# Kernel tuning notes

Measured on AMD Instinct MI355X. Metric: run time of the kernel, lower is better.

## Reference

```python
import jax, jax.numpy as jnp
import numpy as np

# Dims inferred from the module: conv weight (K=3, C_IN=C+1, C_OUT=C)
K_W = 3
C_OUT = 64
C_IN = C_OUT + 1
B, L = 32, 8192
N_STEPS = 8  # fixed-step RK4 stand-in for odeint(rtol=atol=1e-3) over t in [0,1]


def setup_inputs() -> dict:
    key = jax.random.key(0)
    kx, kw = jax.random.split(key)
    x = jax.random.normal(kx, (B, L, C_OUT), dtype=jnp.float32)
    # lecun_uniform: U(-sqrt(3/fan_in), sqrt(3/fan_in)), fan_in = K_W * C_IN
    limit = float(np.sqrt(3.0 / (K_W * C_IN)))
    w = jax.random.uniform(kw, (K_W, C_IN, C_OUT), dtype=jnp.float32,
                           minval=-limit, maxval=limit)
    b = jnp.zeros((C_OUT,), dtype=jnp.float32)
    return {"x": x, "w": w, "b": b}


def _ode_func(y, t, w, b):
    # concat_t: append a constant-t channel -> (B, L, C+1)
    t_chan = jnp.full(y.shape[:-1] + (1,), 1.0, dtype=y.dtype) * t
    z = jnp.concatenate([y, t_chan], axis=-1)
    z = jax.lax.conv_general_dilated(
        z, w, window_strides=(1,), padding="SAME",
        dimension_numbers=("NWC", "WIO", "NWC"))
    return jax.nn.relu(z + b)


def reference(x, w, b):
    h = jnp.float32(1.0 / N_STEPS)

    def step(y, t0):
        k1 = _ode_func(y, t0, w, b)
        k2 = _ode_func(y + 0.5 * h * k1, t0 + 0.5 * h, w, b)
        k3 = _ode_func(y + 0.5 * h * k2, t0 + 0.5 * h, w, b)
        k4 = _ode_func(y + h * k3, t0 + h, w, b)
        y_next = y + (h / 6.0) * (k1 + 2.0 * k2 + 2.0 * k3 + k4)
        return y_next, None

    ts = jnp.arange(N_STEPS, dtype=jnp.float32) * h
    y_final, _ = jax.lax.scan(step, x, ts)
    return y_final
```

## Files before the change

### kernel.cpp

```cpp
#include <hip/hip_runtime.h>
#include <hip/hip_bf16.h>


#define BB 32
#define LL 8192
#define CC 64
#define TILE 64
#define NROW 80
#define BUFR 82
#define ZST 72
#define YST 66
#define CENT_LO 9
#define CENT_HI 72
#define THREADS 256

typedef __attribute__((ext_vector_type(8))) short bf16x8;
typedef __attribute__((ext_vector_type(4))) float f32x4;

__device__ __forceinline__ unsigned short f2bf_u(float f) {
    __hip_bfloat16 h = __float2bfloat16(f);
    return *reinterpret_cast<unsigned short*>(&h);
}

__launch_bounds__(THREADS, 3)
__global__ void step_kernel(const float* __restrict__ y_in, float* __restrict__ y_out,
                            const float* __restrict__ w, const float* __restrict__ bias,
                            float t0, float h)
{
    __shared__ float ys[BUFR * YST];
    __shared__ unsigned short zA[BUFR * ZST];
    __shared__ unsigned short zB[BUFR * ZST];
    __shared__ float wts[3 * CC];
    __shared__ float bs[CC];

    const int tid = threadIdx.x;
    const int b = blockIdx.y;
    const int l0 = blockIdx.x * TILE;
    const int lane = tid & 63;
    const int wv = tid >> 6;
    const int co0 = wv * 16;
    const int g = lane >> 4;
    const int ml = lane & 15;

    bf16x8 bhi[6], blo[6];
#pragma unroll
    for (int c = 0; c < 6; c++) {
        const int kw = c >> 1;
        const int cbase = (c & 1) * 32 + g * 8;
        const float* wp = w + kw * (65 * CC) + cbase * CC + co0 + ml;
#pragma unroll
        for (int j = 0; j < 8; j++) {
            float v = wp[j * CC];
            unsigned short hi = f2bf_u(v);
            float vhi = __uint_as_float(((unsigned)hi) << 16);
            unsigned short lo = f2bf_u(v - vhi);
            bhi[c][j] = (short)hi;
            blo[c][j] = (short)lo;
        }
    }

    if (tid < 3 * CC) wts[tid] = w[(tid >> 6) * (65 * CC) + CC * CC + (tid & 63)];
    if (tid < CC) bs[tid] = bias[tid];

    if (tid < CC) {
        zA[0 * ZST + tid] = 0; zA[81 * ZST + tid] = 0;
        zB[0 * ZST + tid] = 0; zB[81 * ZST + tid] = 0;
    }

    for (int idx = tid; idx < NROW * 16; idx += THREADS) {
        int r = 1 + (idx >> 4);
        int c4 = (idx & 15) * 4;
        int l = l0 - 9 + r;
        float4 v = make_float4(0.f, 0.f, 0.f, 0.f);
        if (l >= 0 && l < LL)
            v = *reinterpret_cast<const float4*>(y_in + ((size_t)b * LL + l) * CC + c4);
        float* yp = &ys[r * YST + c4];
        yp[0] = v.x; yp[1] = v.y; yp[2] = v.z; yp[3] = v.w;
        unsigned short* zp = &zA[r * ZST + c4];
        zp[0] = f2bf_u(v.x); zp[1] = f2bf_u(v.y);
        zp[2] = f2bf_u(v.z); zp[3] = f2bf_u(v.w);
    }
    __syncthreads();

    const float ca0 = h / 6.f, ca1 = h / 3.f;
    const int co = co0 + ml;
    const float w1t = wts[CC + co], w0t = wts[co], w2t = wts[2 * CC + co];
    const float bv = bs[co];

    float accR[5][4];

#pragma unroll 1
    for (int e = 0; e < 4; e++) {
        const unsigned short* zin = (e & 1) ? zB : zA;
        unsigned short* zout = (e & 1) ? zA : zB;
        const float t = t0 + ((e == 0) ? 0.f : (e == 3) ? h : 0.5f * h);
        const float cacc = (e == 0 || e == 3) ? ca0 : ca1;
        const float cuu = (e == 2) ? h : 0.5f * h;

#pragma unroll
        for (int m = 0; m < 5; m++) {
            const int r0 = 1 + 16 * m;
            f32x4 acc = {0.f, 0.f, 0.f, 0.f};
#pragma unroll
            for (int c = 0; c < 6; c++) {
                const int kw = c >> 1;
                const int zoff = (c & 1) * 32 + g * 8;
                const int row = r0 + ml + kw - 1;
                const bf16x8 a =
                    *reinterpret_cast<const bf16x8*>(&zin[row * ZST + zoff]);
                acc = __builtin_amdgcn_mfma_f32_16x16x32_bf16(a, bhi[c], acc, 0, 0, 0);
                acc = __builtin_amdgcn_mfma_f32_16x16x32_bf16(a, blo[c], acc, 0, 0, 0);
            }
#pragma unroll
            for (int i = 0; i < 4; i++) {
                const int rr = r0 + g * 4 + i;
                const int l = l0 - 9 + rr;
                float wt = w1t;
                if (l > 0) wt += w0t;
                if (l < LL - 1) wt += w2t;
                float k = fmaxf(acc[i] + t * wt + bv, 0.f);
                const float yv = ys[rr * YST + co];
                if (e < 3) {
                    float u = yv + cuu * k;
                    if (l < 0 || l >= LL) u = 0.f;
                    zout[rr * ZST + co] = f2bf_u(u);
                }
                accR[m][i] = ((e == 0) ? yv : accR[m][i]) + cacc * k;
            }
        }
        __syncthreads();
    }

#pragma unroll
    for (int m = 0; m < 5; m++) {
#pragma unroll
        for (int i = 0; i < 4; i++) {
            const int rr = 1 + 16 * m + g * 4 + i;
            if (rr >= CENT_LO && rr <= CENT_HI) {
                const int l = l0 - 9 + rr;
                y_out[((size_t)b * LL + l) * CC + co] = accR[m][i];
            }
        }
    }
}

extern "C" void kernel_launch(void* const* d_in, const int* in_sizes, int n_in,
                              void* d_out, int out_size, void* d_ws, size_t ws_size,
                              hipStream_t stream) {
    const float* x = (const float*)d_in[0];
    const float* w = (const float*)d_in[1];
    const float* bias = (const float*)d_in[2];
    float* out = (float*)d_out;
    float* P0 = (float*)d_ws;
    const float h = 1.0f / 8.0f;

    dim3 grid(LL / TILE, BB), block(THREADS);
    for (int s = 0; s < 8; s++) {
        const float* yin = (s == 0) ? x : ((s & 1) ? P0 : out);
        float* yout = (s & 1) ? out : P0;
        step_kernel<<<grid, block, 0, stream>>>(yin, yout, w, bias, s * h, h);
    }
}
```

Before: 700.7 us.

## Enlarge tile, drop bf16 split-precision, keep y in registers

Each block now covers 120 output rows with a 4-row halo instead of 64 with a 9-row halo, which cuts the redundant halo compute and loads. The hi/lo bf16 split of the weights is dropped, so only one bf16 MFMA runs per product, halving MFMA work but lowering precision. The y values stay in registers instead of a shared-memory fp32 buffer. A manual round-to-nearest-even pack writes two channels at once, and edge handling runs only in boundary blocks. The risk is larger numerical error from the single bf16 weights, which may exceed the tolerance.

```diff
diff --git a/kernel.cpp b/kernel.cpp
--- a/kernel.cpp
+++ b/kernel.cpp
@@ -1,145 +1,155 @@
 #include <hip/hip_runtime.h>
-#include <hip/hip_bf16.h>
 
 
 #define BB 32
 #define LL 8192
 #define CC 64
-#define TILE 64
-#define NROW 80
-#define BUFR 82
+#define TILE 120
+#define NBLK 69
+#define BUFR 130
 #define ZST 72
-#define YST 66
-#define CENT_LO 9
-#define CENT_HI 72
 #define THREADS 256
 
 typedef __attribute__((ext_vector_type(8))) short bf16x8;
 typedef __attribute__((ext_vector_type(4))) float f32x4;
 
-__device__ __forceinline__ unsigned short f2bf_u(float f) {
-    __hip_bfloat16 h = __float2bfloat16(f);
-    return *reinterpret_cast<unsigned short*>(&h);
+__device__ __forceinline__ unsigned bf_rne(float f) {
+    unsigned u = __float_as_uint(f);
+    return u + 0x7fffu + ((u >> 16) & 1u);
 }
+__device__ __forceinline__ unsigned pack_bf16(float a, float b) {
+    return (bf_rne(a) >> 16) | (bf_rne(b) & 0xffff0000u);
+}
+__device__ __forceinline__ short bf16_of(float f) { return (short)(bf_rne(f) >> 16); }
 
 __launch_bounds__(THREADS, 3)
 __global__ void step_kernel(const float* __restrict__ y_in, float* __restrict__ y_out,
                             const float* __restrict__ w, const float* __restrict__ bias,
                             float t0, float h)
 {
-    __shared__ float ys[BUFR * YST];
     __shared__ unsigned short zA[BUFR * ZST];
     __shared__ unsigned short zB[BUFR * ZST];
-    __shared__ float wts[3 * CC];
-    __shared__ float bs[CC];
 
     const int tid = threadIdx.x;
     const int b = blockIdx.y;
     const int l0 = blockIdx.x * TILE;
     const int lane = tid & 63;
     const int wv = tid >> 6;
-    const int co0 = wv * 16;
+    const int ch = wv >> 1;
+    const int bset = wv & 1;
     const int g = lane >> 4;
     const int ml = lane & 15;
+    const int co = ch * 32 + 2 * ml;
+    const bool edge = (blockIdx.x == 0) || (blockIdx.x == NBLK - 1);
 
-    bf16x8 bhi[6], blo[6];
+    if (tid < 64) {
+        zA[tid] = 0; zA[129 * ZST + tid] = 0;
+        zB[tid] = 0; zB[129 * ZST + tid] = 0;
+    }
+
+    bf16x8 Bf[6][2];
 #pragma unroll
     for (int c = 0; c < 6; c++) {
-        const int kw = c >> 1;
-        const int cbase = (c & 1) * 32 + g * 8;
-        const float* wp = w + kw * (65 * CC) + cbase * CC + co0 + ml;
+        const float* wp = w + (c >> 1) * (65 * CC) + (((c & 1) * 32) + g * 8) * CC + co;
 #pragma unroll
         for (int j = 0; j < 8; j++) {
-            float v = wp[j * CC];
-            unsigned short hi = f2bf_u(v);
-            float vhi = __uint_as_float(((unsigned)hi) << 16);
-            unsigned short lo = f2bf_u(v - vhi);
-            bhi[c][j] = (short)hi;
-            blo[c][j] = (short)lo;
+            float2 v = *(const float2*)(wp + j * CC);
+            Bf[c][0][j] = bf16_of(v.x);
+            Bf[c][1][j] = bf16_of(v.y);
         }
     }
+    const float2 wt0 = *(const float2*)(w + 0 * (65 * CC) + CC * CC + co);
+    const float2 wt1 = *(const float2*)(w + 1 * (65 * CC) + CC * CC + co);
+    const float2 wt2 = *(const float2*)(w + 2 * (65 * CC) + CC * CC + co);
+    const float2 bv  = *(const float2*)(bias + co);
 
-    if (tid < 3 * CC) wts[tid] = w[(tid >> 6) * (65 * CC) + CC * CC + (tid & 63)];
-    if (tid < CC) bs[tid] = bias[tid];
-
-    if (tid < CC) {
-        zA[0 * ZST + tid] = 0; zA[81 * ZST + tid] = 0;
-        zB[0 * ZST + tid] = 0; zB[81 * ZST + tid] = 0;
-    }
-
-    for (int idx = tid; idx < NROW * 16; idx += THREADS) {
-        int r = 1 + (idx >> 4);
-        int c4 = (idx & 15) * 4;
-        int l = l0 - 9 + r;
-        float4 v = make_float4(0.f, 0.f, 0.f, 0.f);
-        if (l >= 0 && l < LL)
-            v = *reinterpret_cast<const float4*>(y_in + ((size_t)b * LL + l) * CC + c4);
-        float* yp = &ys[r * YST + c4];
-        yp[0] = v.x; yp[1] = v.y; yp[2] = v.z; yp[3] = v.w;
-        unsigned short* zp = &zA[r * ZST + c4];
-        zp[0] = f2bf_u(v.x); zp[1] = f2bf_u(v.y);
-        zp[2] = f2bf_u(v.z); zp[3] = f2bf_u(v.w);
+    float2 yv[4][4];
+#pragma unroll
+    for (int bb = 0; bb < 4; bb++) {
+        const int r0 = (bset * 4 + bb) * 16;
+#pragma unroll
+        for (int i = 0; i < 4; i++) {
+            const int r = r0 + g * 4 + i;
+            const int l = l0 - 4 + r;
+            float2 v = make_float2(0.f, 0.f);
+            if (l >= 0 && l < LL)
+                v = *(const float2*)(y_in + ((size_t)b * LL + l) * CC + co);
+            yv[bb][i] = v;
+            *(unsigned*)&zA[(r + 1) * ZST + co] = pack_bf16(v.x, v.y);
+        }
     }
     __syncthreads();
 
-    const float ca0 = h / 6.f, ca1 = h / 3.f;
-    const int co = co0 + ml;
-    const float w1t = wts[CC + co], w0t = wts[co], w2t = wts[2 * CC + co];
-    const float bv = bs[co];
+    float2 aR[4][4];
+    const float ca[4]  = {h / 6.f, h / 3.f, h / 3.f, h / 6.f};
+    const float cuv[4] = {0.5f * h, 0.5f * h, h, 0.f};
+    const float tof[4] = {0.f, 0.5f * h, 0.5f * h, h};
 
-    float accR[5][4];
-
-#pragma unroll 1
+#pragma unroll
     for (int e = 0; e < 4; e++) {
         const unsigned short* zin = (e & 1) ? zB : zA;
         unsigned short* zout = (e & 1) ? zA : zB;
-        const float t = t0 + ((e == 0) ? 0.f : (e == 3) ? h : 0.5f * h);
-        const float cacc = (e == 0 || e == 3) ? ca0 : ca1;
-        const float cuu = (e == 2) ? h : 0.5f * h;
+        const float t = t0 + tof[e];
+        const float cacc = ca[e], cuu = cuv[e];
+        const float2 tb = {t * (wt0.x + wt1.x + wt2.x) + bv.x,
+                           t * (wt0.y + wt1.y + wt2.y) + bv.y};
 
 #pragma unroll
-        for (int m = 0; m < 5; m++) {
-            const int r0 = 1 + 16 * m;
-            f32x4 acc = {0.f, 0.f, 0.f, 0.f};
+        for (int bb = 0; bb < 4; bb++) {
+            const int r0 = (bset * 4 + bb) * 16;
+            f32x4 acc0 = {0.f, 0.f, 0.f, 0.f};
+            f32x4 acc1 = {0.f, 0.f, 0.f, 0.f};
 #pragma unroll
             for (int c = 0; c < 6; c++) {
-                const int kw = c >> 1;
-                const int zoff = (c & 1) * 32 + g * 8;
-                const int row = r0 + ml + kw - 1;
+                const int br = r0 + ml + (c >> 1);
                 const bf16x8 a =
-                    *reinterpret_cast<const bf16x8*>(&zin[row * ZST + zoff]);
-                acc = __builtin_amdgcn_mfma_f32_16x16x32_bf16(a, bhi[c], acc, 0, 0, 0);
-                acc = __builtin_amdgcn_mfma_f32_16x16x32_bf16(a, blo[c], acc, 0, 0, 0);
+                    *(const bf16x8*)&zin[br * ZST + ((c & 1) * 32) + g * 8];
+                acc0 = __builtin_amdgcn_mfma_f32_16x16x32_bf16(a, Bf[c][0], acc0, 0, 0, 0);
+                acc1 = __builtin_amdgcn_mfma_f32_16x16x32_bf16(a, Bf[c][1], acc1, 0, 0, 0);
             }
 #pragma unroll
             for (int i = 0; i < 4; i++) {
-                const int rr = r0 + g * 4 + i;
-                const int l = l0 - 9 + rr;
-                float wt = w1t;
-                if (l > 0) wt += w0t;
-                if (l < LL - 1) wt += w2t;
-                float k = fmaxf(acc[i] + t * wt + bv, 0.f);
-                const float yv = ys[rr * YST + co];
+                float k0 = acc0[i] + tb.x;
+                float k1 = acc1[i] + tb.y;
+                if (edge) {
+                    const int l = l0 - 4 + r0 + g * 4 + i;
+                    if (l == 0)      { k0 -= t * wt0.x; k1 -= t * wt0.y; }
+                    if (l == LL - 1) { k0 -= t * wt2.x; k1 -= t * wt2.y; }
+                }
+                k0 = fmaxf(k0, 0.f);
+                k1 = fmaxf(k1, 0.f);
+                const float2 y2 = yv[bb][i];
+                if (e == 0) {
+                    aR[bb][i].x = y2.x + cacc * k0;
+                    aR[bb][i].y = y2.y + cacc * k1;
+                } else {
+                    aR[bb][i].x += cacc * k0;
+                    aR[bb][i].y += cacc * k1;
+                }
                 if (e < 3) {
-                    float u = yv + cuu * k;
-                    if (l < 0 || l >= LL) u = 0.f;
-                    zout[rr * ZST + co] = f2bf_u(u);
+                    float u0 = y2.x + cuu * k0;
+                    float u1 = y2.y + cuu * k1;
+                    if (edge) {
+                        const int l = l0 - 4 + r0 + g * 4 + i;
+                        if (l < 0 || l >= LL) { u0 = 0.f; u1 = 0.f; }
+                    }
+                    *(unsigned*)&zout[(r0 + g * 4 + i + 1) * ZST + co] =
+                        pack_bf16(u0, u1);
                 }
-                accR[m][i] = ((e == 0) ? yv : accR[m][i]) + cacc * k;
             }
         }
-        __syncthreads();
+        if (e < 3) __syncthreads();
     }
 
 #pragma unroll
-    for (int m = 0; m < 5; m++) {
+    for (int bb = 0; bb < 4; bb++) {
+        const int r0 = (bset * 4 + bb) * 16;
 #pragma unroll
         for (int i = 0; i < 4; i++) {
-            const int rr = 1 + 16 * m + g * 4 + i;
-            if (rr >= CENT_LO && rr <= CENT_HI) {
-                const int l = l0 - 9 + rr;
-                y_out[((size_t)b * LL + l) * CC + co] = accR[m][i];
-            }
+            const int r = r0 + g * 4 + i;
+            const int l = l0 - 4 + r;
+            if (r >= 4 && r < 124 && l < LL)
+                *(float2*)(y_out + ((size_t)b * LL + l) * CC + co) = aR[bb][i];
         }
     }
 }
@@ -154,7 +164,7 @@
     float* P0 = (float*)d_ws;
     const float h = 1.0f / 8.0f;
 
-    dim3 grid(LL / TILE, BB), block(THREADS);
+    dim3 grid(NBLK, BB), block(THREADS);
     for (int s = 0; s < 8; s++) {
         const float* yin = (s == 0) ? x : ((s & 1) ? P0 : out);
         float* yout = (s & 1) ? out : P0;
```

After: 1.485 ms. 2.12x slower.
